# Optimization experiments

Measured on AMD Instinct MI355X. Metric: run time of the kernel, lower is better.

The kernel has to match this reference:

```python
import jax, jax.numpy as jnp
import numpy as np

# fixed finite-difference stencils (torch cross-correlation taps)
W5 = (1.0/12.0, -8.0/12.0, 0.0, 8.0/12.0, -1.0/12.0)  # five-point, pad=2
W3 = (-0.5, 0.0, 0.5)                                   # three-point, pad=1
P_LIST = np.array([10.0, 8.5, 5.0], dtype=np.float32).reshape(3, 1, 1)


def _circ_deriv(x, axis, taps, pad):
    # torch conv with circular pad: out[i] = sum_k w[k] * x[(i + k - pad) % n]
    # x[(i + k - pad) % n] == roll(x, pad - k)[i]
    out = jnp.zeros_like(x)
    for k, w in enumerate(taps):
        if w != 0.0:
            out = out + w * jnp.roll(x, pad - k, axis=axis)
    return out


def setup_inputs() -> dict:
    key = jax.random.key(0)
    k1, k2, k3, k4 = jax.random.split(key, 4)
    b, si_z, i_y, i_x = 4, 12, 720, 1440
    return {
        "Field": jax.random.normal(k1, (b, si_z, i_y, i_x), dtype=jnp.float32),
        "W": jax.random.normal(k2, (15, 12), dtype=jnp.float32) * 0.02,
        "b_bias": jax.random.normal(k3, (15,), dtype=jnp.float32) * 0.02,
        "thermal_factor": jax.random.normal(k4, (1,), dtype=jnp.float32),
    }


def reference(Field, W, b_bias, thermal_factor):
    b, si_z, i_y, i_x = Field.shape
    s = 4
    i_z = si_z // s  # == 3

    # backbone: 1x1 conv / channel-mixing linear, (b,12,y,x) -> (b,15,y,x)
    ml = jnp.einsum("oc,bcyx->boyx", W, Field) + b_bias[None, :, None, None]
    ml = ml.reshape(b, s + 1, i_z, i_y, i_x)
    ExternalForce = ml[:, :4]           # (b,4,z,y,x)
    o = ml[:, 4:5]                      # (b,1,z,y,x)

    F5 = Field.reshape(b, s, i_z, i_y, i_x)
    u = F5[:, 0:1]
    v = F5[:, 1:2]
    T = F5[:, 2:3]

    Fdx = _circ_deriv(F5, -1, W5, 2)    # d/dx, circular five-point
    Fdy = _circ_deriv(F5, -2, W5, 2)    # d/dy
    Fdz = _circ_deriv(F5, -3, W3, 1)    # d/dz, three-point

    p_list = jnp.asarray(P_LIST)        # (3,1,1) broadcasts over z,y,x
    term3 = thermal_factor[0] * T[:, 0] / p_list * o[:, 0]   # (b,3,y,x)... (b,z=3,y,x)
    phys = jnp.stack([-Fdx[:, 3], -Fdy[:, 3], term3], axis=1)  # (b,3,z,y,x)
    phys = jnp.pad(phys, ((0, 0), (0, 1), (0, 0), (0, 0), (0, 0)))  # -> (b,4,z,y,x)

    xydirection = -u * Fdx - v * Fdy
    PhysicsPart = xydirection - o * Fdz + phys
    Delta = ExternalForce + PhysicsPart
    Field_new = F5 + Delta

    constrain = Fdx[:, 0] + Fdy[:, 1] + _circ_deriv(o[:, 0], -3, W3, 1)

    return (
        Field_new.reshape(b, si_z, i_y, i_x),
        jnp.mean(constrain ** 2),
        jnp.mean(ExternalForce ** 2),
        jnp.mean(PhysicsPart ** 2),
        jnp.mean(xydirection ** 2),
    )
```

## Files before the change

### kernel.cpp

```cpp
#include <hip/hip_runtime.h>

#define IX 1440
#define IY 720
#define NB 4
#define NCH 12
#define PLANE (IY * IX)
#define NOUT (NB * NCH * PLANE)
#define NTHREADS (NB * PLANE / 2)
#define NWG (NTHREADS / 256)
#define SWZ_Q (NWG / 8)
#define SWZ_R (NWG % 8)

typedef float f2v __attribute__((ext_vector_type(2)));

__global__ void zero_ws_kernel(double* ws) {
    if (threadIdx.x < 4) ws[threadIdx.x] = 0.0;
}

__device__ __forceinline__ void ld2(const float* p, float o[2]) {
    const f2v v = *reinterpret_cast<const f2v*>(p);
    o[0] = v.x; o[1] = v.y;
}

__global__ __launch_bounds__(256) void euler_kernel(
    const float* __restrict__ Field,
    const float* __restrict__ W,
    const float* __restrict__ bvec,
    const float* __restrict__ thermal,
    float* __restrict__ out,
    double* __restrict__ ws)
{
    __shared__ float sW[180];
    __shared__ float sB[16];
    __shared__ float sRed[4][4];

    const int t = threadIdx.x;
    if (t < 180) sW[t] = W[t];
    if (t < 15)  sB[t] = bvec[t];
    const float th = thermal[0];
    __syncthreads();

    const int bid = blockIdx.x;
    const int xcd = bid & 7, pos = bid >> 3;
    const int wg  = (xcd < SWZ_R ? xcd * (SWZ_Q + 1)
                                 : SWZ_R * (SWZ_Q + 1) + (xcd - SWZ_R) * SWZ_Q) + pos;

    const int tid = wg * 256 + t;
    const int xi  = tid % 720;
    const int row = tid / 720;
    const int x2  = xi * 2;
    const int y   = row % IY;
    const int b   = row / IY;

    const int xm  = (x2 == 0)      ? IX - 2 : x2 - 2;
    const int xp  = (x2 == IX - 2) ? 0      : x2 + 2;
    const int ym1 = (y == 0)      ? IY - 1       : y - 1;
    const int ym2 = (y < 2)       ? y + IY - 2   : y - 2;
    const int yp1 = (y == IY - 1) ? 0            : y + 1;
    const int yp2 = (y >= IY - 2) ? y - (IY - 2) : y + 2;

    const float* base = Field + (size_t)b * NCH * PLANE;
    const size_t ro = (size_t)y * IX;

    float ctr[12][2];
#pragma unroll
    for (int c = 0; c < 12; ++c) ld2(base + (size_t)c * PLANE + ro + x2, ctr[c]);

    float ml12[3][2];
#pragma unroll
    for (int z = 0; z < 3; ++z) {
#pragma unroll
        for (int j = 0; j < 2; ++j) ml12[z][j] = sB[12 + z];
#pragma unroll
        for (int cc = 0; cc < 12; ++cc) {
            const float wv = sW[(12 + z) * 12 + cc];
#pragma unroll
            for (int j = 0; j < 2; ++j) ml12[z][j] = fmaf(wv, ctr[cc][j], ml12[z][j]);
        }
    }

    float c2 = 0.f, ef2 = 0.f, pp2 = 0.f, xy2 = 0.f;
    float* ob = out + (size_t)b * NCH * PLANE + ro + x2;

#pragma unroll
    for (int z = 0; z < 3; ++z) {
        const int zp = (z == 2) ? 0 : z + 1;
        const int zm = (z == 0) ? 2 : z - 1;
        const float invp = (z == 0) ? 0.1f : (z == 1) ? (1.0f / 8.5f) : 0.2f;

        float fdx9[2], fdy9[2];
        float conz[2];
#pragma unroll
        for (int j = 0; j < 2; ++j) conz[j] = 0.5f * (ml12[zp][j] - ml12[zm][j]);

#pragma unroll
        for (int fi = 0; fi < 4; ++fi) {
            const int f = (fi == 0) ? 3 : fi - 1;
            const int c = f * 3 + z;
            const float* pc = base + (size_t)c * PLANE;

            float vxm[2], vxp[2], vm2[2], vm1[2], vp1[2], vp2[2];
            ld2(pc + ro + xm, vxm);
            ld2(pc + ro + xp, vxp);
            ld2(pc + (size_t)ym2 * IX + x2, vm2);
            ld2(pc + (size_t)ym1 * IX + x2, vm1);
            ld2(pc + (size_t)yp1 * IX + x2, vp1);
            ld2(pc + (size_t)yp2 * IX + x2, vp2);

            float w[6];
            w[0] = vxm[0]; w[1] = vxm[1];
            w[2] = ctr[c][0]; w[3] = ctr[c][1];
            w[4] = vxp[0]; w[5] = vxp[1];

            float fdx[2], fdy[2];
#pragma unroll
            for (int j = 0; j < 2; ++j) {
                fdx[j] = (w[j] - w[j + 4] + 8.0f * (w[j + 3] - w[j + 1])) * (1.0f / 12.0f);
                fdy[j] = (vm2[j] - vp2[j] + 8.0f * (vp1[j] - vm1[j])) * (1.0f / 12.0f);
            }

            float mlc[2];
#pragma unroll
            for (int j = 0; j < 2; ++j) mlc[j] = sB[c];
#pragma unroll
            for (int cc = 0; cc < 12; ++cc) {
                const float wv = sW[c * 12 + cc];
#pragma unroll
                for (int j = 0; j < 2; ++j) mlc[j] = fmaf(wv, ctr[cc][j], mlc[j]);
            }

            if (f == 3) {
#pragma unroll
                for (int j = 0; j < 2; ++j) { fdx9[j] = fdx[j]; fdy9[j] = fdy[j]; }
            }
            if (f == 0) {
#pragma unroll
                for (int j = 0; j < 2; ++j) conz[j] += fdx[j];
            }
            if (f == 1) {
#pragma unroll
                for (int j = 0; j < 2; ++j) conz[j] += fdy[j];
            }

            float st[2];
#pragma unroll
            for (int j = 0; j < 2; ++j) {
                const float fdz = 0.5f * (ctr[f * 3 + zp][j] - ctr[f * 3 + zm][j]);
                const float xyd = -ctr[z][j] * fdx[j] - ctr[3 + z][j] * fdy[j];
                float ph;
                if      (f == 0) ph = -fdx9[j];
                else if (f == 1) ph = -fdy9[j];
                else if (f == 2) ph = th * ctr[6 + z][j] * invp * ml12[z][j];
                else             ph = 0.0f;
                const float phys = xyd - ml12[z][j] * fdz + ph;
                st[j] = ctr[c][j] + mlc[j] + phys;
                ef2 = fmaf(mlc[j],  mlc[j],  ef2);
                pp2 = fmaf(phys,    phys,    pp2);
                xy2 = fmaf(xyd,     xyd,     xy2);
            }
            f2v sv; sv.x = st[0]; sv.y = st[1];
            __builtin_nontemporal_store(sv, reinterpret_cast<f2v*>(ob + (size_t)c * PLANE));
        }

#pragma unroll
        for (int j = 0; j < 2; ++j) c2 = fmaf(conz[j], conz[j], c2);
    }

    float vals[4] = { c2, ef2, pp2, xy2 };
    const int lane = t & 63;
    const int wv   = t >> 6;
#pragma unroll
    for (int i = 0; i < 4; ++i) {
        float v = vals[i];
        for (int off = 32; off > 0; off >>= 1) v += __shfl_down(v, off, 64);
        if (lane == 0) sRed[wv][i] = v;
    }
    __syncthreads();
    if (t < 4) {
        const double s = (double)sRed[0][t] + (double)sRed[1][t]
                       + (double)sRed[2][t] + (double)sRed[3][t];
        atomicAdd(&ws[t], s);
    }
}

__global__ void finalize_kernel(const double* __restrict__ ws, float* __restrict__ out) {
    if (threadIdx.x == 0) {
        out[NOUT + 0] = (float)(ws[0] / (double)(NB * 3 * PLANE));
        out[NOUT + 1] = (float)(ws[1] / (double)NOUT);
        out[NOUT + 2] = (float)(ws[2] / (double)NOUT);
        out[NOUT + 3] = (float)(ws[3] / (double)NOUT);
    }
}

extern "C" void kernel_launch(void* const* d_in, const int* in_sizes, int n_in,
                              void* d_out, int out_size, void* d_ws, size_t ws_size,
                              hipStream_t stream) {
    const float* Field   = (const float*)d_in[0];
    const float* W       = (const float*)d_in[1];
    const float* bvec    = (const float*)d_in[2];
    const float* thermal = (const float*)d_in[3];
    float*  out = (float*)d_out;
    double* ws  = (double*)d_ws;

    zero_ws_kernel<<<1, 64, 0, stream>>>(ws);
    euler_kernel<<<NWG, 256, 0, stream>>>(Field, W, bvec, thermal, out, ws);
    finalize_kernel<<<1, 64, 0, stream>>>(ws, out);
}
```

Before: 123.0 us.

## Stage stencil halos in double-buffered LDS tiles instead of global neighbor loads

Each workgroup now handles a 32x16 spatial tile. For every channel it loads a 20x40 halo tile into shared memory with 16-byte loads, double-buffered so the next channel's load overlaps the current channel's compute. The x/y stencil neighbors are then read from LDS instead of six separate global loads per channel. This cuts redundant global/L2 traffic for halo reads at the cost of twelve barriers per block and extra LDS use, which may lower occupancy.

```diff
diff --git a/kernel.cpp b/kernel.cpp
--- a/kernel.cpp
+++ b/kernel.cpp
@@ -3,15 +3,21 @@
 #define IX 1440
 #define IY 720
 #define NB 4
-#define NCH 12
 #define PLANE (IY * IX)
-#define NOUT (NB * NCH * PLANE)
-#define NTHREADS (NB * PLANE / 2)
-#define NWG (NTHREADS / 256)
+#define NOUT (NB * 12 * PLANE)
+#define TX 32
+#define TY 16
+#define NBX (IX / TX)
+#define NBY (IY / TY)
+#define NWG (NB * NBX * NBY)
 #define SWZ_Q (NWG / 8)
 #define SWZ_R (NWG % 8)
+#define HROWS (TY + 4)
+#define HCOLS 40
+#define TILE4 (HROWS * HCOLS / 4)
 
 typedef float f2v __attribute__((ext_vector_type(2)));
+typedef float f4v __attribute__((ext_vector_type(4)));
 
 __global__ void zero_ws_kernel(double* ws) {
     if (threadIdx.x < 4) ws[threadIdx.x] = 0.0;
@@ -32,39 +38,51 @@
 {
     __shared__ float sW[180];
     __shared__ float sB[16];
+    __shared__ f4v  buf4[2][TILE4];
     __shared__ float sRed[4][4];
 
     const int t = threadIdx.x;
     if (t < 180) sW[t] = W[t];
     if (t < 15)  sB[t] = bvec[t];
     const float th = thermal[0];
-    __syncthreads();
 
     const int bid = blockIdx.x;
     const int xcd = bid & 7, pos = bid >> 3;
     const int wg  = (xcd < SWZ_R ? xcd * (SWZ_Q + 1)
                                  : SWZ_R * (SWZ_Q + 1) + (xcd - SWZ_R) * SWZ_Q) + pos;
 
-    const int tid = wg * 256 + t;
-    const int xi  = tid % 720;
-    const int row = tid / 720;
-    const int x2  = xi * 2;
-    const int y   = row % IY;
-    const int b   = row / IY;
-
-    const int xm  = (x2 == 0)      ? IX - 2 : x2 - 2;
-    const int xp  = (x2 == IX - 2) ? 0      : x2 + 2;
-    const int ym1 = (y == 0)      ? IY - 1       : y - 1;
-    const int ym2 = (y < 2)       ? y + IY - 2   : y - 2;
-    const int yp1 = (y == IY - 1) ? 0            : y + 1;
-    const int yp2 = (y >= IY - 2) ? y - (IY - 2) : y + 2;
-
-    const float* base = Field + (size_t)b * NCH * PLANE;
-    const size_t ro = (size_t)y * IX;
+    const int bx  = wg % NBX;
+    const int tmp = wg / NBX;
+    const int by  = tmp % NBY;
+    const int b   = tmp / NBY;
+    const int x0  = bx * TX, y0 = by * TY;
+
+    const float* base = Field + (size_t)b * 12 * PLANE;
+
+    const bool ldact = (t < TILE4);
+    int loff = 0;
+    if (ldact) {
+        const int r = t / 10, q = t % 10;
+        int gy = y0 + r - 2;  if (gy < 0) gy += IY; else if (gy >= IY) gy -= IY;
+        int gx = x0 - 4 + q * 4; if (gx < 0) gx += IX; else if (gx >= IX) gx -= IX;
+        loff = gy * IX + gx;
+    }
+
+    const int ty  = t >> 4, txi = t & 15;
+    const int yl  = ty + 2;
+    const int xl  = 4 + 2 * txi;
+    const size_t po = (size_t)(y0 + ty) * IX + (x0 + 2 * txi);
+
+    constexpr int ORD[12] = {9, 0, 3, 6, 10, 1, 4, 7, 11, 2, 5, 8};
 
     float ctr[12][2];
 #pragma unroll
-    for (int c = 0; c < 12; ++c) ld2(base + (size_t)c * PLANE + ro + x2, ctr[c]);
+    for (int c = 0; c < 12; ++c) ld2(base + (size_t)c * PLANE + po, ctr[c]);
+
+    f4v r0 = {};
+    if (ldact) r0 = *reinterpret_cast<const f4v*>(base + (size_t)9 * PLANE + loff);
+
+    __syncthreads();
 
     float ml12[3][2];
 #pragma unroll
@@ -79,91 +97,95 @@
         }
     }
 
+    if (ldact) buf4[0][t] = r0;
+    __syncthreads();
+
     float c2 = 0.f, ef2 = 0.f, pp2 = 0.f, xy2 = 0.f;
-    float* ob = out + (size_t)b * NCH * PLANE + ro + x2;
-
-#pragma unroll
-    for (int z = 0; z < 3; ++z) {
+    float fdx9[2], fdy9[2], conz[2];
+    float* ob = out + (size_t)b * 12 * PLANE + po;
+
+#pragma unroll
+    for (int ci = 0; ci < 12; ++ci) {
+        const int c  = ORD[ci];
+        const int f  = c / 3, z = c % 3;
         const int zp = (z == 2) ? 0 : z + 1;
         const int zm = (z == 0) ? 2 : z - 1;
         const float invp = (z == 0) ? 0.1f : (z == 1) ? (1.0f / 8.5f) : 0.2f;
 
-        float fdx9[2], fdy9[2];
-        float conz[2];
-#pragma unroll
-        for (int j = 0; j < 2; ++j) conz[j] = 0.5f * (ml12[zp][j] - ml12[zm][j]);
-
-#pragma unroll
-        for (int fi = 0; fi < 4; ++fi) {
-            const int f = (fi == 0) ? 3 : fi - 1;
-            const int c = f * 3 + z;
-            const float* pc = base + (size_t)c * PLANE;
-
-            float vxm[2], vxp[2], vm2[2], vm1[2], vp1[2], vp2[2];
-            ld2(pc + ro + xm, vxm);
-            ld2(pc + ro + xp, vxp);
-            ld2(pc + (size_t)ym2 * IX + x2, vm2);
-            ld2(pc + (size_t)ym1 * IX + x2, vm1);
-            ld2(pc + (size_t)yp1 * IX + x2, vp1);
-            ld2(pc + (size_t)yp2 * IX + x2, vp2);
-
-            float w[6];
-            w[0] = vxm[0]; w[1] = vxm[1];
-            w[2] = ctr[c][0]; w[3] = ctr[c][1];
-            w[4] = vxp[0]; w[5] = vxp[1];
-
-            float fdx[2], fdy[2];
+        f4v rn = {};
+        if (ci < 11 && ldact)
+            rn = *reinterpret_cast<const f4v*>(base + (size_t)ORD[ci + 1] * PLANE + loff);
+
+        const float* fb = reinterpret_cast<const float*>(buf4[ci & 1]);
+
+        const f2v wa = *reinterpret_cast<const f2v*>(&fb[yl * HCOLS + xl - 2]);
+        const f2v wb = *reinterpret_cast<const f2v*>(&fb[yl * HCOLS + xl]);
+        const f2v wc = *reinterpret_cast<const f2v*>(&fb[yl * HCOLS + xl + 2]);
+        const f2v m2 = *reinterpret_cast<const f2v*>(&fb[(yl - 2) * HCOLS + xl]);
+        const f2v m1 = *reinterpret_cast<const f2v*>(&fb[(yl - 1) * HCOLS + xl]);
+        const f2v p1 = *reinterpret_cast<const f2v*>(&fb[(yl + 1) * HCOLS + xl]);
+        const f2v p2 = *reinterpret_cast<const f2v*>(&fb[(yl + 2) * HCOLS + xl]);
+
+        float fdx[2], fdy[2];
+        fdx[0] = (wa.x - wc.x + 8.0f * (wb.y - wa.y)) * (1.0f / 12.0f);
+        fdx[1] = (wa.y - wc.y + 8.0f * (wc.x - wb.x)) * (1.0f / 12.0f);
+        fdy[0] = (m2.x - p2.x + 8.0f * (p1.x - m1.x)) * (1.0f / 12.0f);
+        fdy[1] = (m2.y - p2.y + 8.0f * (p1.y - m1.y)) * (1.0f / 12.0f);
+
+        float mlc[2];
+#pragma unroll
+        for (int j = 0; j < 2; ++j) mlc[j] = sB[c];
+#pragma unroll
+        for (int cc = 0; cc < 12; ++cc) {
+            const float wv = sW[c * 12 + cc];
+#pragma unroll
+            for (int j = 0; j < 2; ++j) mlc[j] = fmaf(wv, ctr[cc][j], mlc[j]);
+        }
+
+        if (f == 3) {
 #pragma unroll
             for (int j = 0; j < 2; ++j) {
-                fdx[j] = (w[j] - w[j + 4] + 8.0f * (w[j + 3] - w[j + 1])) * (1.0f / 12.0f);
-                fdy[j] = (vm2[j] - vp2[j] + 8.0f * (vp1[j] - vm1[j])) * (1.0f / 12.0f);
+                fdx9[j] = fdx[j]; fdy9[j] = fdy[j];
+                conz[j] = 0.5f * (ml12[zp][j] - ml12[zm][j]);
             }
-
-            float mlc[2];
-#pragma unroll
-            for (int j = 0; j < 2; ++j) mlc[j] = sB[c];
-#pragma unroll
-            for (int cc = 0; cc < 12; ++cc) {
-                const float wv = sW[c * 12 + cc];
-#pragma unroll
-                for (int j = 0; j < 2; ++j) mlc[j] = fmaf(wv, ctr[cc][j], mlc[j]);
-            }
-
-            if (f == 3) {
-#pragma unroll
-                for (int j = 0; j < 2; ++j) { fdx9[j] = fdx[j]; fdy9[j] = fdy[j]; }
-            }
-            if (f == 0) {
-#pragma unroll
-                for (int j = 0; j < 2; ++j) conz[j] += fdx[j];
-            }
-            if (f == 1) {
-#pragma unroll
-                for (int j = 0; j < 2; ++j) conz[j] += fdy[j];
-            }
-
-            float st[2];
-#pragma unroll
-            for (int j = 0; j < 2; ++j) {
-                const float fdz = 0.5f * (ctr[f * 3 + zp][j] - ctr[f * 3 + zm][j]);
-                const float xyd = -ctr[z][j] * fdx[j] - ctr[3 + z][j] * fdy[j];
-                float ph;
-                if      (f == 0) ph = -fdx9[j];
-                else if (f == 1) ph = -fdy9[j];
-                else if (f == 2) ph = th * ctr[6 + z][j] * invp * ml12[z][j];
-                else             ph = 0.0f;
-                const float phys = xyd - ml12[z][j] * fdz + ph;
-                st[j] = ctr[c][j] + mlc[j] + phys;
-                ef2 = fmaf(mlc[j],  mlc[j],  ef2);
-                pp2 = fmaf(phys,    phys,    pp2);
-                xy2 = fmaf(xyd,     xyd,     xy2);
-            }
-            f2v sv; sv.x = st[0]; sv.y = st[1];
-            __builtin_nontemporal_store(sv, reinterpret_cast<f2v*>(ob + (size_t)c * PLANE));
-        }
-
-#pragma unroll
-        for (int j = 0; j < 2; ++j) c2 = fmaf(conz[j], conz[j], c2);
+        }
+        if (f == 0) {
+#pragma unroll
+            for (int j = 0; j < 2; ++j) conz[j] += fdx[j];
+        }
+        if (f == 1) {
+#pragma unroll
+            for (int j = 0; j < 2; ++j) conz[j] += fdy[j];
+        }
+
+        float st[2];
+#pragma unroll
+        for (int j = 0; j < 2; ++j) {
+            const float fdz = 0.5f * (ctr[f * 3 + zp][j] - ctr[f * 3 + zm][j]);
+            const float xyd = -ctr[z][j] * fdx[j] - ctr[3 + z][j] * fdy[j];
+            float ph;
+            if      (f == 0) ph = -fdx9[j];
+            else if (f == 1) ph = -fdy9[j];
+            else if (f == 2) ph = th * ctr[6 + z][j] * invp * ml12[z][j];
+            else             ph = 0.0f;
+            const float phys = xyd - ml12[z][j] * fdz + ph;
+            st[j] = ctr[c][j] + mlc[j] + phys;
+            ef2 = fmaf(mlc[j], mlc[j], ef2);
+            pp2 = fmaf(phys,   phys,   pp2);
+            xy2 = fmaf(xyd,    xyd,    xy2);
+        }
+        f2v sv; sv.x = st[0]; sv.y = st[1];
+        __builtin_nontemporal_store(sv, reinterpret_cast<f2v*>(ob + (size_t)c * PLANE));
+
+        if (f == 2) {
+#pragma unroll
+            for (int j = 0; j < 2; ++j) c2 = fmaf(conz[j], conz[j], c2);
+        }
+
+        if (ci < 11) {
+            if (ldact) buf4[(ci + 1) & 1][t] = rn;
+            __syncthreads();
+        }
     }
 
     float vals[4] = { c2, ef2, pp2, xy2 };
```

After: 127.1 us. +3.4%, slower.
